# Kernel tuning notes

Measured on AMD Instinct MI355X. Metric: run time of the kernel, lower is better.

## Reference

```python
import jax, jax.numpy as jnp
import numpy as np

V = 50257  # vocab_size
E = 512    # embed_dim
H = 512    # hidden_dim
N = 32     # batch
T = 128    # sequence length


def setup_inputs() -> dict:
    key = jax.random.key(0)
    ks = jax.random.split(key, 8)
    s = 1.0 / np.sqrt(H)  # PyTorch GRUCell init range
    words = jax.random.randint(ks[0], (N, T), 0, V)
    hidden_state = jnp.zeros((N, H), jnp.float32)
    embed_W = jax.random.uniform(ks[1], (V, E), jnp.float32, -1.0, 1.0)  # init_weights uniform_(-1,1)
    W_ih = jax.random.uniform(ks[2], (3 * H, E), jnp.float32, -s, s)
    W_hh = jax.random.uniform(ks[3], (3 * H, H), jnp.float32, -s, s)
    b_ih = jax.random.uniform(ks[4], (3 * H,), jnp.float32, -s, s)
    b_hh = jax.random.uniform(ks[5], (3 * H,), jnp.float32, -s, s)
    emit_W = jax.random.uniform(ks[6], (V, H), jnp.float32, -1.0, 1.0)
    emit_b = jnp.zeros((V,), jnp.float32)
    return {"words": words, "hidden_state": hidden_state, "embed_W": embed_W,
            "W_ih": W_ih, "W_hh": W_hh, "b_ih": b_ih, "b_hh": b_hh,
            "emit_W": emit_W, "emit_b": emit_b}


def _gru_cell(x, h, W_ih, W_hh, b_ih, b_hh):
    gi = x @ W_ih.T + b_ih          # [N, 3H]
    gh = h @ W_hh.T + b_hh          # [N, 3H]
    i_r, i_z, i_n = jnp.split(gi, 3, axis=-1)
    h_r, h_z, h_n = jnp.split(gh, 3, axis=-1)
    r = jax.nn.sigmoid(i_r + h_r)
    z = jax.nn.sigmoid(i_z + h_z)
    n = jnp.tanh(i_n + r * h_n)
    return (1.0 - z) * n + z * h


def reference(words, hidden_state, embed_W, W_ih, W_hh, b_ih, b_hh, emit_W, emit_b):
    emb = embed_W[words[:, :-1]]        # [N, T-1, E]
    xs = jnp.swapaxes(emb, 0, 1)        # [T-1, N, E]
    targets = words[:, 1:].T            # [T-1, N]

    def step(h, inp):
        x, widx = inp
        h_new = _gru_cell(x, h, W_ih, W_hh, b_ih, b_hh)
        logits = h_new @ emit_W.T + emit_b                 # [N, V]
        logp = jax.nn.log_softmax(logits, axis=-1)
        ll = jnp.take_along_axis(logp, widx[:, None], axis=1)[:, 0]  # [N]
        return h_new, ll

    h_final, lls = jax.lax.scan(step, hidden_state, (xs, targets))
    emit_marginal = lls.sum(axis=0) / (T - 1)              # [N]
    return emit_marginal, h_final
```

## Files before the change

kernel.cpp:

```cpp
#include <hip/hip_runtime.h>
#include <math.h>

#define V_SIZE 50257
#define EMB 512
#define HID 512
#define NB 32
#define TT 128
#define NSTEP 127
#define G3H 1536
#define MROWS 4064
#define MPAD 4096
#define VPAD 50304
#define NT_V 393
#define NBLK_GRU 32
#define FLAG_STRIDE 32
#define NTILE (16 * NT_V)
#define NWORKER 448
#define SMEM_BYTES 77312

typedef __attribute__((ext_vector_type(4))) float f32x4;
typedef __attribute__((ext_vector_type(8))) __bf16 bf16x8;
typedef __attribute__((ext_vector_type(4))) __bf16 bf16x4;

struct u128 { unsigned long long a, b; };

__device__ __forceinline__ void async16(const __bf16* g, __bf16* l) {
    __builtin_amdgcn_global_load_lds(
        (const __attribute__((address_space(1))) void*)g,
        (__attribute__((address_space(3))) void*)l, 16, 0, 0);
}


__global__ void k_prep_emit(const float* __restrict__ src, __bf16* __restrict__ dst) {
    size_t total4 = (size_t)VPAD * 512 / 4;
    size_t real4  = (size_t)V_SIZE * 512 / 4;
    for (size_t i4 = (size_t)blockIdx.x * blockDim.x + threadIdx.x; i4 < total4;
         i4 += (size_t)gridDim.x * blockDim.x) {
        float4 v = (i4 < real4) ? ((const float4*)src)[i4] : make_float4(0.f,0.f,0.f,0.f);
        bf16x4 o = {(__bf16)v.x, (__bf16)v.y, (__bf16)v.z, (__bf16)v.w};
        ((bf16x4*)dst)[i4] = o;
    }
}

__global__ void k_prep_wih(const float* __restrict__ src, __bf16* __restrict__ dst) {
    size_t total4 = (size_t)G3H * 512 / 4;
    for (size_t i4 = (size_t)blockIdx.x * blockDim.x + threadIdx.x; i4 < total4;
         i4 += (size_t)gridDim.x * blockDim.x) {
        float4 v = ((const float4*)src)[i4];
        bf16x4 o = {(__bf16)v.x, (__bf16)v.y, (__bf16)v.z, (__bf16)v.w};
        ((bf16x4*)dst)[i4] = o;
    }
}

__global__ void k_prep_x(const int* __restrict__ words, const float* __restrict__ embed,
                         __bf16* __restrict__ Xb, __bf16* __restrict__ Hs) {
    int s = blockIdx.x;
    int n = blockIdx.y;
    int tid = threadIdx.x;
    if (s < NSTEP) {
        int w = words[n * TT + s];
        size_t row = (size_t)(s * NB + n);
        const float4* src = (const float4*)(embed + (size_t)w * EMB);
        bf16x4* dst = (bf16x4*)(Xb + row * EMB);
        for (int c = tid; c < EMB / 4; c += 128) {
            float4 v = src[c];
            bf16x4 o = {(__bf16)v.x, (__bf16)v.y, (__bf16)v.z, (__bf16)v.w};
            dst[c] = o;
        }
    } else {
        size_t row = (size_t)(MROWS + n);
        bf16x4 z = {(__bf16)0.f, (__bf16)0.f, (__bf16)0.f, (__bf16)0.f};
        for (int c = tid; c < EMB / 4; c += 128) {
            ((bf16x4*)(Xb + row * EMB))[c] = z;
            ((bf16x4*)(Hs + row * HID))[c] = z;
        }
    }
}

__global__ void k_prep_h0(const float* __restrict__ h0, __bf16* __restrict__ Hbuf,
                          int* __restrict__ ctrl) {
    int b = blockIdx.x;
    if (b < NB) {
        for (int k = threadIdx.x; k < HID; k += 256)
            Hbuf[b * HID + k] = (__bf16)h0[b * HID + k];
    } else {
        for (int k = threadIdx.x; k < 2048; k += 256) ctrl[k] = 0;
    }
}


__device__ __forceinline__ void mm128(const __bf16* __restrict__ A,
                                      const __bf16* __restrict__ B,
                                      int mBase, int nBase, f32x4 acc[4][4],
                                      __bf16* As, __bf16* Bs) {
    const int tid = threadIdx.x;
    const int lane = tid & 63, wave = tid >> 6;
    const int wm = wave >> 1, wn = wave & 1;
    const int lane15 = lane & 15, quad = lane >> 4;
    for (int kc = 0; kc < 512; kc += 64) {
        __syncthreads();
#pragma unroll
        for (int i = 0; i < 4; ++i) {
            int c = (wave * 4 + i) * 64 + lane;
            int row = c >> 3, ci = c & 7;
            int cis = ci ^ (row & 7);
            async16(A + (size_t)(mBase + row) * 512 + kc + (cis << 3), As + (wave * 4 + i) * 512);
            async16(B + (size_t)(nBase + row) * 512 + kc + (cis << 3), Bs + (wave * 4 + i) * 512);
        }
        __syncthreads();
#pragma unroll
        for (int ks = 0; ks < 64; ks += 32) {
            bf16x8 a4[4], b4[4];
#pragma unroll
            for (int mi = 0; mi < 4; ++mi) {
                int row = wm * 64 + mi * 16 + lane15;
                int L = (ks >> 3) + quad;
                a4[mi] = *(const bf16x8*)(As + row * 64 + ((L ^ (row & 7)) << 3));
            }
#pragma unroll
            for (int ni = 0; ni < 4; ++ni) {
                int row = wn * 64 + ni * 16 + lane15;
                int L = (ks >> 3) + quad;
                b4[ni] = *(const bf16x8*)(Bs + row * 64 + ((L ^ (row & 7)) << 3));
            }
#pragma unroll
            for (int mi = 0; mi < 4; ++mi)
#pragma unroll
                for (int ni = 0; ni < 4; ++ni)
                    acc[mi][ni] = __builtin_amdgcn_mfma_f32_16x16x32_bf16(
                        a4[mi], b4[ni], acc[mi][ni], 0, 0, 0);
        }
    }
}

__global__ __launch_bounds__(256) void k_gemm_gi(const __bf16* __restrict__ Xb,
                                                 const __bf16* __restrict__ Wihb,
                                                 const float* __restrict__ b_ih,
                                                 const float* __restrict__ b_hh,
                                                 float* __restrict__ gi) {
    __shared__ __align__(16) __bf16 As[128 * 64];
    __shared__ __align__(16) __bf16 Bs[128 * 64];
    f32x4 acc[4][4];
    f32x4 z = {0.f, 0.f, 0.f, 0.f};
#pragma unroll
    for (int mi = 0; mi < 4; ++mi)
#pragma unroll
        for (int ni = 0; ni < 4; ++ni) acc[mi][ni] = z;
    int mBase = blockIdx.x * 128, nBase = blockIdx.y * 128;
    mm128(Xb, Wihb, mBase, nBase, acc, As, Bs);
    const int tid = threadIdx.x, lane = tid & 63, wave = tid >> 6;
    const int wm = wave >> 1, wn = wave & 1, lane15 = lane & 15, quad = lane >> 4;
#pragma unroll
    for (int ni = 0; ni < 4; ++ni) {
        int col = nBase + wn * 64 + ni * 16 + lane15;
        float bias = b_ih[col] + (col < 1024 ? b_hh[col] : 0.0f);
#pragma unroll
        for (int mi = 0; mi < 4; ++mi) {
            int rowb = wm * 64 + mi * 16 + quad * 4;
#pragma unroll
            for (int r = 0; r < 4; ++r) {
                int m = mBase + rowb + r;
                gi[(size_t)m * G3H + col] = acc[mi][ni][r] + bias;
            }
        }
    }
}

#define CREDp(w,g,m,jc) Cred[(((w)*3+(g))*32+(m))*17+(jc)]

__global__ __launch_bounds__(256, 2) void k_fused(
    const float* __restrict__ W_hh, const float* __restrict__ gi,
    const float* __restrict__ b_hh, const float* __restrict__ h0,
    __bf16* __restrict__ Hbuf,
    __bf16* __restrict__ Hs,
    float* __restrict__ Hfin,
    const __bf16* __restrict__ Wemb,
    const float* __restrict__ emit_b,
    float2* __restrict__ partials,
    int* __restrict__ ctrl)
{
    __shared__ __align__(16) char smem[SMEM_BYTES];
    __shared__ int tShare;
    const int tid = threadIdx.x;
    const int lane = tid & 63, wave = tid >> 6;
    const int lane15 = lane & 15, quad = lane >> 4;
    int* ticket   = ctrl;
    int* progress = ctrl + 32;
    int* flags    = ctrl + 64;

    if (blockIdx.x < NBLK_GRU) {
        const int blk = blockIdx.x;
        const int j0 = blk * 16;
        __bf16* Wl  = (__bf16*)smem;
        float* Cred = (float*)(smem + 49920);
        __bf16 (*HbO)[16] = (__bf16(*)[16])(smem + 76032);

        for (int idx = tid; idx < 48 * 128; idx += 256) {
            int rr = idx >> 7, k4 = (idx & 127) << 2;
            int g = rr >> 4, jc = rr & 15;
            float4 v = *(const float4*)(W_hh + (size_t)(g * 512 + j0 + jc) * 512 + k4);
            __bf16* d = &Wl[rr * 520 + k4];
            d[0] = (__bf16)v.x; d[1] = (__bf16)v.y; d[2] = (__bf16)v.z; d[3] = (__bf16)v.w;
        }

        const int m0 = tid >> 4, jc0 = tid & 15;
        const int m1 = m0 + 16;
        const float bhn = b_hh[1024 + j0 + jc0];
        const int k0 = wave * 128;
        float hp0 = h0[(size_t)m0 * HID + j0 + jc0];
        float hp1 = h0[(size_t)m1 * HID + j0 + jc0];

        float ir0, iz0, in0, ir1, iz1, in1;
        {
            const float* g0 = gi + (size_t)m0 * G3H + j0 + jc0;
            const float* g1 = gi + (size_t)m1 * G3H + j0 + jc0;
            ir0 = g0[0]; iz0 = g0[512]; in0 = g0[1024];
            ir1 = g1[0]; iz1 = g1[512]; in1 = g1[1024];
        }
        __syncthreads();

        for (int s = 0; s < NSTEP; ++s) {
            const __bf16* hb = Hbuf + (size_t)(s & 1) * NB * HID;
            unsigned long long hq[2][4][2];
#pragma unroll
            for (int mt = 0; mt < 2; ++mt)
#pragma unroll
                for (int kk = 0; kk < 4; ++kk) {
                    const unsigned long long* pp = (const unsigned long long*)
                        (hb + (size_t)(mt * 16 + lane15) * HID + k0 + kk * 32 + quad * 8);
                    hq[mt][kk][0] = __hip_atomic_load(pp, __ATOMIC_RELAXED, __HIP_MEMORY_SCOPE_AGENT);
                    hq[mt][kk][1] = __hip_atomic_load(pp + 1, __ATOMIC_RELAXED, __HIP_MEMORY_SCOPE_AGENT);
                }

            f32x4 acc[2][3];
            f32x4 zz = {0.f, 0.f, 0.f, 0.f};
#pragma unroll
            for (int mt = 0; mt < 2; ++mt)
#pragma unroll
                for (int g = 0; g < 3; ++g) acc[mt][g] = zz;
#pragma unroll
            for (int kk = 0; kk < 4; ++kk) {
                int ks = kk * 32;
                bf16x8 a0 = __builtin_bit_cast(bf16x8, u128{hq[0][kk][0], hq[0][kk][1]});
                bf16x8 a1 = __builtin_bit_cast(bf16x8, u128{hq[1][kk][0], hq[1][kk][1]});
#pragma unroll
                for (int g = 0; g < 3; ++g) {
                    bf16x8 b4 = *(const bf16x8*)(&Wl[(g * 16 + lane15) * 520 + k0 + ks + quad * 8]);
                    acc[0][g] = __builtin_amdgcn_mfma_f32_16x16x32_bf16(a0, b4, acc[0][g], 0, 0, 0);
                    acc[1][g] = __builtin_amdgcn_mfma_f32_16x16x32_bf16(a1, b4, acc[1][g], 0, 0, 0);
                }
            }
#pragma unroll
            for (int mt = 0; mt < 2; ++mt)
#pragma unroll
                for (int g = 0; g < 3; ++g)
#pragma unroll
                    for (int r = 0; r < 4; ++r)
                        CREDp(wave, g, mt * 16 + quad * 4 + r, lane15) = acc[mt][g][r];
            __syncthreads();

            {
                float gr = CREDp(0,0,m0,jc0) + CREDp(1,0,m0,jc0) + CREDp(2,0,m0,jc0) + CREDp(3,0,m0,jc0);
                float gz = CREDp(0,1,m0,jc0) + CREDp(1,1,m0,jc0) + CREDp(2,1,m0,jc0) + CREDp(3,1,m0,jc0);
                float gn = CREDp(0,2,m0,jc0) + CREDp(1,2,m0,jc0) + CREDp(2,2,m0,jc0) + CREDp(3,2,m0,jc0);
                float r = 1.f / (1.f + expf(-(ir0 + gr)));
                float zg = 1.f / (1.f + expf(-(iz0 + gz)));
                float nn = tanhf(in0 + r * (gn + bhn));
                hp0 = (1.f - zg) * nn + zg * hp0;
                HbO[m0][jc0] = (__bf16)hp0;
            }
            {
                float gr = CREDp(0,0,m1,jc0) + CREDp(1,0,m1,jc0) + CREDp(2,0,m1,jc0) + CREDp(3,0,m1,jc0);
                float gz = CREDp(0,1,m1,jc0) + CREDp(1,1,m1,jc0) + CREDp(2,1,m1,jc0) + CREDp(3,1,m1,jc0);
                float gn = CREDp(0,2,m1,jc0) + CREDp(1,2,m1,jc0) + CREDp(2,2,m1,jc0) + CREDp(3,2,m1,jc0);
                float r = 1.f / (1.f + expf(-(ir1 + gr)));
                float zg = 1.f / (1.f + expf(-(iz1 + gz)));
                float nn = tanhf(in1 + r * (gn + bhn));
                hp1 = (1.f - zg) * nn + zg * hp1;
                HbO[m1][jc0] = (__bf16)hp1;
            }
            __syncthreads();

            if (tid < 128) {
                int m = tid >> 2, g4 = tid & 3;
                unsigned long long v0 = *(const unsigned short*)&HbO[m][g4 * 4 + 0];
                unsigned long long v1 = *(const unsigned short*)&HbO[m][g4 * 4 + 1];
                unsigned long long v2 = *(const unsigned short*)&HbO[m][g4 * 4 + 2];
                unsigned long long v3 = *(const unsigned short*)&HbO[m][g4 * 4 + 3];
                unsigned long long pk = v0 | (v1 << 16) | (v2 << 32) | (v3 << 48);
                unsigned long long* dst = (unsigned long long*)
                    (Hbuf + (size_t)((s + 1) & 1) * NB * HID + (size_t)m * HID + j0 + g4 * 4);
                __hip_atomic_store(dst, pk, __ATOMIC_RELAXED, __HIP_MEMORY_SCOPE_AGENT);
                unsigned long long* dst2 = (unsigned long long*)
                    (Hs + (size_t)(s * NB + m) * HID + j0 + g4 * 4);
                __hip_atomic_store(dst2, pk, __ATOMIC_RELAXED, __HIP_MEMORY_SCOPE_AGENT);
            }

            __builtin_amdgcn_s_waitcnt(0x0f70);
            __syncthreads();

            if (tid == 0)
                __hip_atomic_store(&flags[blk * FLAG_STRIDE], s + 1,
                                   __ATOMIC_RELAXED, __HIP_MEMORY_SCOPE_AGENT);

            float nir0, niz0, nin0, nir1, niz1, nin1;
            if (s + 1 < NSTEP) {
                const float* g0 = gi + (size_t)((s + 1) * NB + m0) * G3H + j0 + jc0;
                const float* g1 = gi + (size_t)((s + 1) * NB + m1) * G3H + j0 + jc0;
                nir0 = g0[0]; niz0 = g0[512]; nin0 = g0[1024];
                nir1 = g1[0]; niz1 = g1[512]; nin1 = g1[1024];
            } else {
                nir0 = niz0 = nin0 = nir1 = niz1 = nin1 = 0.f;
            }

            if (tid < NBLK_GRU) {
                while (__hip_atomic_load(&flags[tid * FLAG_STRIDE],
                                         __ATOMIC_RELAXED, __HIP_MEMORY_SCOPE_AGENT) < s + 1)
                    __builtin_amdgcn_s_sleep(1);
            }
            __syncthreads();

            if (blk == 0 && tid == 0)
                __hip_atomic_store(progress, s + 1,
                                   __ATOMIC_RELAXED, __HIP_MEMORY_SCOPE_AGENT);

            ir0 = nir0; iz0 = niz0; in0 = nin0;
            ir1 = nir1; iz1 = niz1; in1 = nin1;
        }

        Hfin[(size_t)m0 * HID + j0 + jc0] = hp0;
        Hfin[(size_t)m1 * HID + j0 + jc0] = hp1;

    } else {
        __bf16* As = (__bf16*)smem;
        __bf16* Bs = (__bf16*)(smem + 32768);
        const float NINF = -__builtin_inff();

        for (;;) {
            if (tid == 0) {
                int t = __hip_atomic_fetch_add(ticket, 1, __ATOMIC_RELAXED,
                                               __HIP_MEMORY_SCOPE_AGENT);
                tShare = t;
                if (t < NTILE) {
                    int mc = t / NT_V;
                    int need = (mc == 15) ? NSTEP : 8 * (mc + 1);
                    while (__hip_atomic_load(progress, __ATOMIC_RELAXED,
                                             __HIP_MEMORY_SCOPE_AGENT) < need)
                        __builtin_amdgcn_s_sleep(32);
                }
            }
            __syncthreads();
            int t = tShare;
            if (t >= NTILE) break;
            int mc = t / NT_V;
            int nT = t - mc * NT_V;
            int mBase = mc * 256, nBase = nT * 128;

            f32x4 acc[4][8];
            f32x4 z = {0.f, 0.f, 0.f, 0.f};
#pragma unroll
            for (int mi = 0; mi < 4; ++mi)
#pragma unroll
                for (int ni = 0; ni < 8; ++ni) acc[mi][ni] = z;

            for (int kc = 0; kc < 512; kc += 64) {
                __syncthreads();
#pragma unroll
                for (int i = 0; i < 8; ++i) {
                    int c = (wave * 8 + i) * 64 + lane;
                    int row = c >> 3, ci = c & 7;
                    int cis = ci ^ (row & 7);
                    async16(Hs + (size_t)(mBase + row) * 512 + kc + (cis << 3),
                            As + (wave * 8 + i) * 512);
                }
#pragma unroll
                for (int i = 0; i < 4; ++i) {
                    int c = (wave * 4 + i) * 64 + lane;
                    int row = c >> 3, ci = c & 7;
                    int cis = ci ^ (row & 7);
                    async16(Wemb + (size_t)(nBase + row) * 512 + kc + (cis << 3),
                            Bs + (wave * 4 + i) * 512);
                }
                __syncthreads();
#pragma unroll
                for (int ks = 0; ks < 64; ks += 32) {
                    int L = (ks >> 3) + quad;
                    bf16x8 a4[4], b4[8];
#pragma unroll
                    for (int mi = 0; mi < 4; ++mi) {
                        int row = wave * 64 + mi * 16 + lane15;
                        a4[mi] = *(const bf16x8*)(As + row * 64 + ((L ^ (row & 7)) << 3));
                    }
#pragma unroll
                    for (int ni = 0; ni < 8; ++ni) {
                        int row = ni * 16 + lane15;
                        b4[ni] = *(const bf16x8*)(Bs + row * 64 + ((L ^ (row & 7)) << 3));
                    }
#pragma unroll
                    for (int mi = 0; mi < 4; ++mi)
#pragma unroll
                        for (int ni = 0; ni < 8; ++ni)
                            acc[mi][ni] = __builtin_amdgcn_mfma_f32_16x16x32_bf16(
                                a4[mi], b4[ni], acc[mi][ni], 0, 0, 0);
                }
            }

            float bv[8];
            bool valid[8];
#pragma unroll
            for (int ni = 0; ni < 8; ++ni) {
                int col = nBase + ni * 16 + lane15;
                valid[ni] = (col < V_SIZE);
                bv[ni] = valid[ni] ? emit_b[col] : 0.0f;
            }
#pragma unroll
            for (int mi = 0; mi < 4; ++mi) {
#pragma unroll
                for (int r = 0; r < 4; ++r) {
                    float vals[8];
                    float vmax = NINF;
#pragma unroll
                    for (int ni = 0; ni < 8; ++ni) {
                        float v = acc[mi][ni][r] + bv[ni];
                        if (!valid[ni]) v = NINF;
                        vals[ni] = v;
                        vmax = fmaxf(vmax, v);
                    }
#pragma unroll
                    for (int off = 1; off < 16; off <<= 1)
                        vmax = fmaxf(vmax, __shfl_xor(vmax, off));
                    float ssum = 0.f;
#pragma unroll
                    for (int ni = 0; ni < 8; ++ni) ssum += expf(vals[ni] - vmax);
#pragma unroll
                    for (int off = 1; off < 16; off <<= 1) ssum += __shfl_xor(ssum, off);
                    if (lane15 == 0) {
                        int m = mBase + wave * 64 + mi * 16 + quad * 4 + r;
                        partials[(size_t)m * NT_V + nT] = make_float2(vmax, ssum);
                    }
                }
            }
        }
    }
}

__global__ __launch_bounds__(128) void k_row_ll(const float2* __restrict__ partials,
                                                const __bf16* __restrict__ Hs,
                                                const __bf16* __restrict__ Wemb,
                                                const float* __restrict__ emit_b,
                                                const int* __restrict__ words,
                                                float* __restrict__ lls) {
    int s = blockIdx.x, n = blockIdx.y;
    int m = s * NB + n;
    int tid = threadIdx.x;
    int lane = tid & 63, w = tid >> 6;
    __shared__ float sm[2], ss[2], sd[2];
    const float2* prow = partials + (size_t)m * NT_V;
    float M = -__builtin_inff();
    for (int i = tid; i < NT_V; i += 128) M = fmaxf(M, prow[i].x);
#pragma unroll
    for (int off = 1; off < 64; off <<= 1) M = fmaxf(M, __shfl_xor(M, off));
    if (lane == 0) sm[w] = M;
    __syncthreads();
    M = fmaxf(sm[0], sm[1]);
    float S = 0.f;
    for (int i = tid; i < NT_V; i += 128) {
        float2 p = prow[i];
        S += p.y * expf(p.x - M);
    }
#pragma unroll
    for (int off = 1; off < 64; off <<= 1) S += __shfl_xor(S, off);
    if (lane == 0) ss[w] = S;
    __syncthreads();
    S = ss[0] + ss[1];
    int tw = words[n * TT + s + 1];
    float d = 0.f;
    const __bf16* hr = Hs + (size_t)m * HID;
    const __bf16* wr = Wemb + (size_t)tw * HID;
    for (int k = tid; k < HID; k += 128) d += (float)hr[k] * (float)wr[k];
#pragma unroll
    for (int off = 1; off < 64; off <<= 1) d += __shfl_xor(d, off);
    if (lane == 0) sd[w] = d;
    __syncthreads();
    if (tid == 0) {
        float dt = sd[0] + sd[1];
        lls[m] = dt + emit_b[tw] - (M + logf(S));
    }
}

__global__ __launch_bounds__(128) void k_final(const float* __restrict__ lls,
                                               const float* __restrict__ Hfin,
                                               float* __restrict__ out) {
    int n = blockIdx.x;
    int tid = threadIdx.x;
    float s = 0.f;
    for (int i = tid; i < NSTEP; i += 128) s += lls[i * NB + n];
#pragma unroll
    for (int off = 1; off < 64; off <<= 1) s += __shfl_xor(s, off);
    __shared__ float t2[2];
    if ((tid & 63) == 0) t2[tid >> 6] = s;
    __syncthreads();
    if (tid == 0) out[n] = (t2[0] + t2[1]) / (float)NSTEP;
    for (int i = tid; i < HID; i += 128) out[NB + n * HID + i] = Hfin[(size_t)n * HID + i];
}

extern "C" void kernel_launch(void* const* d_in, const int* in_sizes, int n_in,
                              void* d_out, int out_size, void* d_ws, size_t ws_size,
                              hipStream_t stream) {
    const int*   words   = (const int*)d_in[0];
    const float* hidden0 = (const float*)d_in[1];
    const float* embed_W = (const float*)d_in[2];
    const float* W_ih    = (const float*)d_in[3];
    const float* W_hh    = (const float*)d_in[4];
    const float* b_ih    = (const float*)d_in[5];
    const float* b_hh    = (const float*)d_in[6];
    const float* emit_W  = (const float*)d_in[7];
    const float* emit_b  = (const float*)d_in[8];
    float* out = (float*)d_out;

    char* p = (char*)d_ws;
    auto alloc = [&](size_t bytes) {
        void* r = (void*)p;
        p += (bytes + 255) & ~(size_t)255;
        return r;
    };
    __bf16* emit_Wb = (__bf16*)alloc((size_t)VPAD * 512 * 2);
    __bf16* Xb      = (__bf16*)alloc((size_t)MPAD * 512 * 2);
    __bf16* Wihb    = (__bf16*)alloc((size_t)G3H * 512 * 2);
    float*  gi      = (float*)alloc((size_t)MPAD * G3H * 4);
    __bf16* Hs      = (__bf16*)alloc((size_t)MPAD * 512 * 2);
    __bf16* Hbuf    = (__bf16*)alloc((size_t)2 * NB * HID * 2);
    float*  Hfin    = (float*)alloc((size_t)NB * HID * 4);
    float2* partials= (float2*)alloc((size_t)MPAD * NT_V * 8);
    float*  lls     = (float*)alloc((size_t)MROWS * 4);
    int*    ctrl    = (int*)alloc(2048 * 4);

    k_prep_emit<<<4096, 256, 0, stream>>>(emit_W, emit_Wb);
    k_prep_x<<<dim3(128, 32), 128, 0, stream>>>(words, embed_W, Xb, Hs);
    k_prep_wih<<<768, 256, 0, stream>>>(W_ih, Wihb);
    k_prep_h0<<<NB + 1, 256, 0, stream>>>(hidden0, Hbuf, ctrl);

    k_gemm_gi<<<dim3(32, 12), 256, 0, stream>>>(Xb, Wihb, b_ih, b_hh, gi);

    k_fused<<<NBLK_GRU + NWORKER, 256, 0, stream>>>(
        W_hh, gi, b_hh, hidden0, Hbuf, Hs, Hfin, emit_Wb, emit_b, partials, ctrl);

    k_row_ll<<<dim3(NSTEP, 32), 128, 0, stream>>>(partials, Hs, emit_Wb, emit_b, words, lls);
    k_final<<<32, 128, 0, stream>>>(lls, Hfin, out);
}
```

Measured before the change: 878.8 us.

## Replace per-step GRU barrier with tagged hidden-state words and fuse emit conversion

GRU blocks now publish each hidden-state pair as a 64-bit word that carries its step number. Consumers spin until every word they read has the expected tag, which replaces the all-block flag barrier on every step. Progress flags for the worker GEMM are only published every 8 steps, and workers poll the per-block flags directly. The separate emit_W fp32-to-bf16 kernel is folded into the worker blocks, which convert it while the GRU runs, then join the GEMM tile queue after a global counter barrier. This doubles the hidden-state traffic and adds spin-read retries in exchange for removing the per-step global synchronization and one kernel launch.

Result: slower. 1.105 ms (+25.7%).

```diff
diff --git a/kernel.cpp b/kernel.cpp
--- a/kernel.cpp
+++ b/kernel.cpp
@@ -21,8 +21,8 @@
 typedef __attribute__((ext_vector_type(4))) float f32x4;
 typedef __attribute__((ext_vector_type(8))) __bf16 bf16x8;
 typedef __attribute__((ext_vector_type(4))) __bf16 bf16x4;
-
-struct u128 { unsigned long long a, b; };
+typedef __attribute__((ext_vector_type(4))) unsigned int u32x4;
+typedef unsigned long long ull;
 
 __device__ __forceinline__ void async16(const __bf16* g, __bf16* l) {
     __builtin_amdgcn_global_load_lds(
@@ -30,17 +30,13 @@
         (__attribute__((address_space(3))) void*)l, 16, 0, 0);
 }
 
-
-__global__ void k_prep_emit(const float* __restrict__ src, __bf16* __restrict__ dst) {
-    size_t total4 = (size_t)VPAD * 512 / 4;
-    size_t real4  = (size_t)V_SIZE * 512 / 4;
-    for (size_t i4 = (size_t)blockIdx.x * blockDim.x + threadIdx.x; i4 < total4;
-         i4 += (size_t)gridDim.x * blockDim.x) {
-        float4 v = (i4 < real4) ? ((const float4*)src)[i4] : make_float4(0.f,0.f,0.f,0.f);
-        bf16x4 o = {(__bf16)v.x, (__bf16)v.y, (__bf16)v.z, (__bf16)v.w};
-        ((bf16x4*)dst)[i4] = o;
-    }
-}
+__device__ __forceinline__ unsigned int packbf2(float a, float b) {
+    __bf16 x = (__bf16)a, y = (__bf16)b;
+    unsigned short ux = __builtin_bit_cast(unsigned short, x);
+    unsigned short uy = __builtin_bit_cast(unsigned short, y);
+    return (unsigned int)ux | ((unsigned int)uy << 16);
+}
+
 
 __global__ void k_prep_wih(const float* __restrict__ src, __bf16* __restrict__ dst) {
     size_t total4 = (size_t)G3H * 512 / 4;
@@ -77,17 +73,20 @@
     }
 }
 
-__global__ void k_prep_h0(const float* __restrict__ h0, __bf16* __restrict__ Hbuf,
+__global__ void k_prep_h0(const float* __restrict__ h0, ull* __restrict__ Htag,
                           int* __restrict__ ctrl) {
     int b = blockIdx.x;
+    int tid = threadIdx.x;
     if (b < NB) {
-        for (int k = threadIdx.x; k < HID; k += 256)
-            Hbuf[b * HID + k] = (__bf16)h0[b * HID + k];
+        int c = tid;
+        float v0 = h0[(size_t)b * HID + 2 * c];
+        float v1 = h0[(size_t)b * HID + 2 * c + 1];
+        Htag[(size_t)b * 256 + c] = (ull)packbf2(v0, v1);
+        Htag[(size_t)(NB + b) * 256 + c] = 0xFFFFFFFF00000000ull;
     } else {
-        for (int k = threadIdx.x; k < 2048; k += 256) ctrl[k] = 0;
-    }
-}
-
+        for (int k = tid; k < 2048; k += 256) ctrl[k] = 0;
+    }
+}
 
 __device__ __forceinline__ void mm128(const __bf16* __restrict__ A,
                                       const __bf16* __restrict__ B,
@@ -171,22 +170,23 @@
 __global__ __launch_bounds__(256, 2) void k_fused(
     const float* __restrict__ W_hh, const float* __restrict__ gi,
     const float* __restrict__ b_hh, const float* __restrict__ h0,
-    __bf16* __restrict__ Hbuf,
+    ull* __restrict__ Htag,
     __bf16* __restrict__ Hs,
     float* __restrict__ Hfin,
-    const __bf16* __restrict__ Wemb,
+    const float* __restrict__ emit_W,
+    __bf16* __restrict__ Wemb,
     const float* __restrict__ emit_b,
     float2* __restrict__ partials,
     int* __restrict__ ctrl)
 {
     __shared__ __align__(16) char smem[SMEM_BYTES];
-    __shared__ int tShare;
+    __shared__ int tShare, needShare;
     const int tid = threadIdx.x;
     const int lane = tid & 63, wave = tid >> 6;
     const int lane15 = lane & 15, quad = lane >> 4;
-    int* ticket   = ctrl;
-    int* progress = ctrl + 32;
-    int* flags    = ctrl + 64;
+    int* ticket  = ctrl;
+    int* convCnt = ctrl + 32;
+    int* flags   = ctrl + 64;
 
     if (blockIdx.x < NBLK_GRU) {
         const int blk = blockIdx.x;
@@ -209,28 +209,39 @@
         const int k0 = wave * 128;
         float hp0 = h0[(size_t)m0 * HID + j0 + jc0];
         float hp1 = h0[(size_t)m1 * HID + j0 + jc0];
-
-        float ir0, iz0, in0, ir1, iz1, in1;
-        {
-            const float* g0 = gi + (size_t)m0 * G3H + j0 + jc0;
-            const float* g1 = gi + (size_t)m1 * G3H + j0 + jc0;
-            ir0 = g0[0]; iz0 = g0[512]; in0 = g0[1024];
-            ir1 = g1[0]; iz1 = g1[512]; in1 = g1[1024];
-        }
         __syncthreads();
 
         for (int s = 0; s < NSTEP; ++s) {
-            const __bf16* hb = Hbuf + (size_t)(s & 1) * NB * HID;
-            unsigned long long hq[2][4][2];
-#pragma unroll
-            for (int mt = 0; mt < 2; ++mt)
-#pragma unroll
-                for (int kk = 0; kk < 4; ++kk) {
-                    const unsigned long long* pp = (const unsigned long long*)
-                        (hb + (size_t)(mt * 16 + lane15) * HID + k0 + kk * 32 + quad * 8);
-                    hq[mt][kk][0] = __hip_atomic_load(pp, __ATOMIC_RELAXED, __HIP_MEMORY_SCOPE_AGENT);
-                    hq[mt][kk][1] = __hip_atomic_load(pp + 1, __ATOMIC_RELAXED, __HIP_MEMORY_SCOPE_AGENT);
-                }
+            const float* g0 = gi + (size_t)(s * NB + m0) * G3H + j0 + jc0;
+            const float* g1 = gi + (size_t)(s * NB + m1) * G3H + j0 + jc0;
+            float ir0 = g0[0], iz0 = g0[512], in0 = g0[1024];
+            float ir1 = g1[0], iz1 = g1[512], in1 = g1[1024];
+
+            const ull* hb = Htag + (size_t)(s & 1) * NB * 256;
+            ull hq[2][4][4];
+            const unsigned want = (unsigned)s;
+            bool ok;
+            do {
+#pragma unroll
+                for (int mt = 0; mt < 2; ++mt)
+#pragma unroll
+                    for (int kk = 0; kk < 4; ++kk) {
+                        const ull* p = hb + (size_t)(mt * 16 + lane15) * 256
+                                       + ((k0 + kk * 32 + quad * 8) >> 1);
+#pragma unroll
+                        for (int i = 0; i < 4; ++i)
+                            hq[mt][kk][i] = __hip_atomic_load(
+                                p + i, __ATOMIC_RELAXED, __HIP_MEMORY_SCOPE_AGENT);
+                    }
+                ok = true;
+#pragma unroll
+                for (int mt = 0; mt < 2; ++mt)
+#pragma unroll
+                    for (int kk = 0; kk < 4; ++kk)
+#pragma unroll
+                        for (int i = 0; i < 4; ++i)
+                            ok = ok && ((unsigned)(hq[mt][kk][i] >> 32) == want);
+            } while (!ok);
 
             f32x4 acc[2][3];
             f32x4 zz = {0.f, 0.f, 0.f, 0.f};
@@ -241,8 +252,12 @@
 #pragma unroll
             for (int kk = 0; kk < 4; ++kk) {
                 int ks = kk * 32;
-                bf16x8 a0 = __builtin_bit_cast(bf16x8, u128{hq[0][kk][0], hq[0][kk][1]});
-                bf16x8 a1 = __builtin_bit_cast(bf16x8, u128{hq[1][kk][0], hq[1][kk][1]});
+                u32x4 w0 = {(unsigned)hq[0][kk][0], (unsigned)hq[0][kk][1],
+                            (unsigned)hq[0][kk][2], (unsigned)hq[0][kk][3]};
+                u32x4 w1 = {(unsigned)hq[1][kk][0], (unsigned)hq[1][kk][1],
+                            (unsigned)hq[1][kk][2], (unsigned)hq[1][kk][3]};
+                bf16x8 a0 = __builtin_bit_cast(bf16x8, w0);
+                bf16x8 a1 = __builtin_bit_cast(bf16x8, w1);
 #pragma unroll
                 for (int g = 0; g < 3; ++g) {
                     bf16x8 b4 = *(const bf16x8*)(&Wl[(g * 16 + lane15) * 520 + k0 + ks + quad * 8]);
@@ -281,57 +296,70 @@
             }
             __syncthreads();
 
+            {
+                int m = tid >> 3, c8 = tid & 7;
+                unsigned short u0 = __builtin_bit_cast(unsigned short, HbO[m][2 * c8]);
+                unsigned short u1 = __builtin_bit_cast(unsigned short, HbO[m][2 * c8 + 1]);
+                unsigned pair = (unsigned)u0 | ((unsigned)u1 << 16);
+                ull pk = (ull)pair | ((ull)(unsigned)(s + 1) << 32);
+                __hip_atomic_store(Htag + (size_t)((s + 1) & 1) * NB * 256
+                                        + (size_t)m * 256 + blk * 8 + c8,
+                                   pk, __ATOMIC_RELAXED, __HIP_MEMORY_SCOPE_AGENT);
+            }
             if (tid < 128) {
                 int m = tid >> 2, g4 = tid & 3;
-                unsigned long long v0 = *(const unsigned short*)&HbO[m][g4 * 4 + 0];
-                unsigned long long v1 = *(const unsigned short*)&HbO[m][g4 * 4 + 1];
-                unsigned long long v2 = *(const unsigned short*)&HbO[m][g4 * 4 + 2];
-                unsigned long long v3 = *(const unsigned short*)&HbO[m][g4 * 4 + 3];
-                unsigned long long pk = v0 | (v1 << 16) | (v2 << 32) | (v3 << 48);
-                unsigned long long* dst = (unsigned long long*)
-                    (Hbuf + (size_t)((s + 1) & 1) * NB * HID + (size_t)m * HID + j0 + g4 * 4);
-                __hip_atomic_store(dst, pk, __ATOMIC_RELAXED, __HIP_MEMORY_SCOPE_AGENT);
-                unsigned long long* dst2 = (unsigned long long*)
-                    (Hs + (size_t)(s * NB + m) * HID + j0 + g4 * 4);
-                __hip_atomic_store(dst2, pk, __ATOMIC_RELAXED, __HIP_MEMORY_SCOPE_AGENT);
-            }
-
-            __builtin_amdgcn_s_waitcnt(0x0f70);
-            __syncthreads();
-
-            if (tid == 0)
-                __hip_atomic_store(&flags[blk * FLAG_STRIDE], s + 1,
-                                   __ATOMIC_RELAXED, __HIP_MEMORY_SCOPE_AGENT);
-
-            float nir0, niz0, nin0, nir1, niz1, nin1;
-            if (s + 1 < NSTEP) {
-                const float* g0 = gi + (size_t)((s + 1) * NB + m0) * G3H + j0 + jc0;
-                const float* g1 = gi + (size_t)((s + 1) * NB + m1) * G3H + j0 + jc0;
-                nir0 = g0[0]; niz0 = g0[512]; nin0 = g0[1024];
-                nir1 = g1[0]; niz1 = g1[512]; nin1 = g1[1024];
-            } else {
-                nir0 = niz0 = nin0 = nir1 = niz1 = nin1 = 0.f;
-            }
-
-            if (tid < NBLK_GRU) {
-                while (__hip_atomic_load(&flags[tid * FLAG_STRIDE],
-                                         __ATOMIC_RELAXED, __HIP_MEMORY_SCOPE_AGENT) < s + 1)
-                    __builtin_amdgcn_s_sleep(1);
-            }
-            __syncthreads();
-
-            if (blk == 0 && tid == 0)
-                __hip_atomic_store(progress, s + 1,
-                                   __ATOMIC_RELAXED, __HIP_MEMORY_SCOPE_AGENT);
-
-            ir0 = nir0; iz0 = niz0; in0 = nin0;
-            ir1 = nir1; iz1 = niz1; in1 = nin1;
+                ull v0 = __builtin_bit_cast(unsigned short, HbO[m][g4 * 4 + 0]);
+                ull v1 = __builtin_bit_cast(unsigned short, HbO[m][g4 * 4 + 1]);
+                ull v2 = __builtin_bit_cast(unsigned short, HbO[m][g4 * 4 + 2]);
+                ull v3 = __builtin_bit_cast(unsigned short, HbO[m][g4 * 4 + 3]);
+                ull pk = v0 | (v1 << 16) | (v2 << 32) | (v3 << 48);
+                __hip_atomic_store((ull*)(Hs + (size_t)(s * NB + m) * HID + j0 + g4 * 4),
+                                   pk, __ATOMIC_RELAXED, __HIP_MEMORY_SCOPE_AGENT);
+            }
+
+            if (((s & 7) == 7) || s == NSTEP - 1) {
+                __builtin_amdgcn_s_waitcnt(0x0f70);
+                __syncthreads();
+                if (tid == 0)
+                    __hip_atomic_store(&flags[blk * FLAG_STRIDE], s + 1,
+                                       __ATOMIC_RELAXED, __HIP_MEMORY_SCOPE_AGENT);
+            }
         }
 
         Hfin[(size_t)m0 * HID + j0 + jc0] = hp0;
         Hfin[(size_t)m1 * HID + j0 + jc0] = hp1;
-
+        __syncthreads();
+        if (tid == 0) {
+            while (__hip_atomic_load(convCnt, __ATOMIC_RELAXED,
+                                     __HIP_MEMORY_SCOPE_AGENT) < NWORKER)
+                __builtin_amdgcn_s_sleep(8);
+        }
+        __syncthreads();
     } else {
+        size_t totalq = (size_t)VPAD * 512 / 4;
+        size_t realq  = (size_t)V_SIZE * 512 / 4;
+        for (size_t i = (size_t)(blockIdx.x - NBLK_GRU) * 256 + tid; i < totalq;
+             i += (size_t)NWORKER * 256) {
+            ull pk = 0;
+            if (i < realq) {
+                float4 v = ((const float4*)emit_W)[i];
+                pk = (ull)packbf2(v.x, v.y) | ((ull)packbf2(v.z, v.w) << 32);
+            }
+            __hip_atomic_store((ull*)Wemb + i, pk,
+                               __ATOMIC_RELAXED, __HIP_MEMORY_SCOPE_AGENT);
+        }
+        __builtin_amdgcn_s_waitcnt(0x0f70);
+        __syncthreads();
+        if (tid == 0) {
+            __hip_atomic_fetch_add(convCnt, 1, __ATOMIC_RELAXED, __HIP_MEMORY_SCOPE_AGENT);
+            while (__hip_atomic_load(convCnt, __ATOMIC_RELAXED,
+                                     __HIP_MEMORY_SCOPE_AGENT) < NWORKER)
+                __builtin_amdgcn_s_sleep(8);
+        }
+        __syncthreads();
+    }
+
+    {
         __bf16* As = (__bf16*)smem;
         __bf16* Bs = (__bf16*)(smem + 32768);
         const float NINF = -__builtin_inff();
@@ -341,17 +369,20 @@
                 int t = __hip_atomic_fetch_add(ticket, 1, __ATOMIC_RELAXED,
                                                __HIP_MEMORY_SCOPE_AGENT);
                 tShare = t;
-                if (t < NTILE) {
-                    int mc = t / NT_V;
-                    int need = (mc == 15) ? NSTEP : 8 * (mc + 1);
-                    while (__hip_atomic_load(progress, __ATOMIC_RELAXED,
-                                             __HIP_MEMORY_SCOPE_AGENT) < need)
-                        __builtin_amdgcn_s_sleep(32);
-                }
+                int mc = t / NT_V;
+                needShare = (mc >= 15) ? NSTEP : 8 * (mc + 1);
             }
             __syncthreads();
             int t = tShare;
             if (t >= NTILE) break;
+            int need = needShare;
+            if (tid < NBLK_GRU) {
+                while (__hip_atomic_load(&flags[tid * FLAG_STRIDE],
+                                         __ATOMIC_RELAXED, __HIP_MEMORY_SCOPE_AGENT) < need)
+                    __builtin_amdgcn_s_sleep(16);
+            }
+            __syncthreads();
+
             int mc = t / NT_V;
             int nT = t - mc * NT_V;
             int mBase = mc * 256, nBase = nT * 128;
@@ -529,21 +560,20 @@
     __bf16* Wihb    = (__bf16*)alloc((size_t)G3H * 512 * 2);
     float*  gi      = (float*)alloc((size_t)MPAD * G3H * 4);
     __bf16* Hs      = (__bf16*)alloc((size_t)MPAD * 512 * 2);
-    __bf16* Hbuf    = (__bf16*)alloc((size_t)2 * NB * HID * 2);
+    ull*    Htag    = (ull*)alloc((size_t)2 * NB * 256 * 8);
     float*  Hfin    = (float*)alloc((size_t)NB * HID * 4);
     float2* partials= (float2*)alloc((size_t)MPAD * NT_V * 8);
     float*  lls     = (float*)alloc((size_t)MROWS * 4);
     int*    ctrl    = (int*)alloc(2048 * 4);
 
-    k_prep_emit<<<4096, 256, 0, stream>>>(emit_W, emit_Wb);
     k_prep_x<<<dim3(128, 32), 128, 0, stream>>>(words, embed_W, Xb, Hs);
     k_prep_wih<<<768, 256, 0, stream>>>(W_ih, Wihb);
-    k_prep_h0<<<NB + 1, 256, 0, stream>>>(hidden0, Hbuf, ctrl);
+    k_prep_h0<<<NB + 1, 256, 0, stream>>>(hidden0, Htag, ctrl);
 
     k_gemm_gi<<<dim3(32, 12), 256, 0, stream>>>(Xb, Wihb, b_ih, b_hh, gi);
 
     k_fused<<<NBLK_GRU + NWORKER, 256, 0, stream>>>(
-        W_hh, gi, b_hh, hidden0, Hbuf, Hs, Hfin, emit_Wb, emit_b, partials, ctrl);
+        W_hh, gi, b_hh, hidden0, Htag, Hs, Hfin, emit_W, emit_Wb, emit_b, partials, ctrl);
 
     k_row_ll<<<dim3(NSTEP, 32), 128, 0, stream>>>(partials, Hs, emit_Wb, emit_b, words, lls);
     k_final<<<32, 128, 0, stream>>>(lls, Hfin, out);
```
